# Optimization experiments

Hardware: AMD Instinct MI355X
Metric: run time of the kernel (lower is better)

The kernel has to match this reference:

```python
import jax, jax.numpy as jnp
import numpy as np


def setup_inputs() -> dict:
    key = jax.random.key(0)
    N0, N1, N2, E0, E1 = 40000, 8000, 2000, 128000, 32000
    IN, HID = 512, 256
    ks = iter(jax.random.split(key, 40))
    def nk():
        return next(ks)
    def lin_w(shape):
        fan_in = shape[1]
        return jax.random.uniform(nk(), shape, jnp.float32, -1.0, 1.0) / np.sqrt(fan_in)
    inp = {}
    inp["x"] = jax.random.normal(nk(), (N0, IN), jnp.float32)
    inp["ppr"] = jax.random.uniform(nk(), (N1, N1), jnp.float32) / N1  # ~row-stochastic PPR
    inp["src0"] = jax.random.randint(nk(), (E0,), 0, N0)
    inp["dst0"] = jax.random.randint(nk(), (E0,), 0, N1)
    inp["src1"] = jax.random.randint(nk(), (E1,), 0, N1)
    inp["dst1"] = jax.random.randint(nk(), (E1,), 0, N2)
    inp["n1"] = N1
    inp["n2"] = N2
    # SAGEConv layer 0 (in->hid) and layer 1 (hid->hid); lin_l has bias, lin_r does not (PyG default)
    inp["Wl0"] = lin_w((HID, IN)); inp["bl0"] = jnp.zeros((HID,), jnp.float32); inp["Wr0"] = lin_w((HID, IN))
    inp["Wl1"] = lin_w((HID, HID)); inp["bl1"] = jnp.zeros((HID,), jnp.float32); inp["Wr1"] = lin_w((HID, HID))
    # self.linear = [Linear(IN,IN)+ReLU, Linear(IN,HID)]
    inp["Wa"] = lin_w((IN, IN)); inp["ba"] = jnp.zeros((IN,), jnp.float32)
    inp["Wb"] = lin_w((HID, IN)); inp["bb"] = jnp.zeros((HID,), jnp.float32)
    # lin1 / lin2 (no bias)
    inp["W1"] = lin_w((HID, HID)); inp["W2"] = lin_w((HID, HID))
    # proj = MLP(HID, HID, HID)
    inp["Wp1"] = lin_w((HID, HID)); inp["bp1"] = jnp.zeros((HID,), jnp.float32)
    inp["Wp2"] = lin_w((HID, HID)); inp["bp2"] = jnp.zeros((HID,), jnp.float32)
    # clf = MLP(HID, 32, 1)
    inp["Wc1"] = lin_w((32, HID)); inp["bc1"] = jnp.zeros((32,), jnp.float32)
    inp["Wc2"] = lin_w((1, 32)); inp["bc2"] = jnp.zeros((1,), jnp.float32)
    return inp


def reference(x, ppr, Wl0, bl0, Wr0, Wl1, bl1, Wr1, Wa, ba, Wb, bb,
              W1, W2, Wp1, bp1, Wp2, bp2, Wc1, bc1, Wc2, bc2,
              src0, dst0, src1, dst1, n1, n2):
    EPS = 1e-12
    def l2n(v):
        return v / jnp.maximum(jnp.linalg.norm(v, axis=-1, keepdims=True), EPS)
    def sage(h_src, h_tgt, src, dst, Wl, bl, Wr, n_tgt):
        msg = h_src[src]  # [E, d] gather
        s = jax.ops.segment_sum(msg, dst, num_segments=n_tgt)
        cnt = jax.ops.segment_sum(jnp.ones((dst.shape[0],), h_src.dtype), dst, num_segments=n_tgt)
        agg = s / jnp.maximum(cnt, 1.0)[:, None]  # scatter-mean
        return agg @ Wl.T + bl + h_tgt @ Wr.T
    # --- GraphSAGE encoder (eval mode: dropout no-op) ---
    h = x
    h = sage(h, h[:n1], src0, dst0, Wl0, bl0, Wr0, n1)
    h = jax.nn.relu(h)
    h = sage(h, h[:n2], src1, dst1, Wl1, bl1, Wr1, n2)
    ebds = jax.nn.log_softmax(h, axis=-1)  # output_type 'ebds' != 'ebd' -> log_softmax path
    # --- divergence loss ---
    o1 = l2n(ebds @ W1.T)
    o2 = l2n(ebds @ W2.T)
    div_loss = jnp.mean(jnp.sum((o1 - o2) ** 2, axis=-1))
    # --- PPR branch ---
    xp = ppr[:n1, :n1] @ x[:n1]              # [n1, IN]
    xp = jax.nn.relu(xp @ Wa.T + ba)         # linear[0]
    xp = ppr[:n2, :n2] @ xp[:n2]             # [n2, IN]
    xp = xp @ Wb.T + bb                      # linear[1] -> [n2, HID]
    g1 = l2n(ebds)
    g2 = l2n(xp)
    def proj(v):
        return jax.nn.relu(v @ Wp1.T + bp1) @ Wp2.T + bp2
    def clf(v):
        return jax.nn.relu(v @ Wc1.T + bc1) @ Wc2.T + bc2
    l1 = clf(proj(g1))  # [n2, 1]
    l2_ = clf(proj(g2))  # [n2, 1]
    logits_pair = jnp.concatenate([l1, l2_], axis=-1)  # [n2, 2]
    return logits_pair, div_loss
```

## Files before the change

kernel.cpp:

```cpp
#include <hip/hip_runtime.h>


typedef unsigned short ushort;
typedef __attribute__((ext_vector_type(8))) short short8;
typedef __attribute__((ext_vector_type(4))) float float4v;
typedef __attribute__((ext_vector_type(4))) float f32x4;
typedef __attribute__((ext_vector_type(2))) float f32x2;
typedef __attribute__((ext_vector_type(8))) unsigned short us8;
typedef __attribute__((ext_vector_type(4))) unsigned short us4;
typedef __attribute__((ext_vector_type(2))) unsigned short us2;

__device__ __forceinline__ ushort bf16_rne(float v) {
    unsigned u = __float_as_uint(v);
    u += 0x7fffu + ((u >> 16) & 1u);
    return (ushort)(u >> 16);
}
__device__ __forceinline__ float bf16_f32(ushort h) {
    return __uint_as_float((unsigned)h << 16);
}

constexpr long ZCNT0 = 0;
constexpr long ZCNT1 = 8000;
constexpr long ELL0  = 10240;
constexpr long ELL1  = 522240;
constexpr long H1F   = 650240;
constexpr long H2F   = 2714624;
constexpr long DIVCF = 3238912;
constexpr long XPBF  = 4287488;
constexpr long PB2   = 4811776;
constexpr long PART  = 5860352;
constexpr long FEND  = 10054656;
constexpr long U_PPRB  = 0;
constexpr long U_PPR2B = 16777216;
constexpr long U_XTB   = 20971520;
constexpr long U_XPATB = 25165824;
constexpr long U_A0    = 26214400;
constexpr long U_A1    = 38600704;
constexpr long U_ESPL  = 40697856;
constexpr long U_XPS   = 41746432;
constexpr long U_SPLT  = 43843584;
constexpr long U_TSPL  = 45940736;
constexpr long U_WC0   = 48037888;
constexpr long U_WC1   = 48431104;
constexpr long U_BD    = 48693248;
constexpr long U_WAD   = 48955392;
constexpr long U_WBD   = 49479680;
constexpr long U_WP1D  = 49741824;
constexpr long U_WP2D  = 49872896;
constexpr long U_XB    = 50003968;

struct GemmDesc {
    const ushort* A; const ushort* B;
    float* Cf; ushort* Cs; ushort* Ct;
    const float* bias;
    int K, lda, ldb, ldc;
    int ldso, nsplit, msplit, ldt;
    int gx, gy, kchunk;
    long slabsize;
    int flags;
};

__device__ __forceinline__ void run_gemm(const GemmDesc& d, int f,
                                         ushort* As, ushort* Bs)
{
    const int tid = threadIdx.x;
    const int lane = tid & 63, wave = tid >> 6;
    const int wm = (wave >> 1) * 64, wn = (wave & 1) * 64;
    const int lr = lane & 15, quad = lane >> 4;

    int per = d.gx * d.gy;
    int z = f / per;
    int rem = f - z * per;
    if (d.flags & 8) {
        int c = rem & 7, j = rem >> 3;
        rem = c * (per >> 3) + j;
    }
    int by = rem / d.gx, bx = rem - by * d.gx;
    const int bm = by * 128, bn = bx * 128;
    const int kbeg = z * d.kchunk;
    int kend = kbeg + d.kchunk; if (kend > d.K) kend = d.K;

    float4v acc[4][4] = {{{0.f, 0.f, 0.f, 0.f}}};

    for (int k0 = kbeg; k0 < kend; k0 += 128) {
#pragma unroll
        for (int issue = 0; issue < 8; ++issue) {
            int c = issue * 256 + tid;
            int r = c >> 4, p = c & 15;
            int kk = (p ^ (r & 15)) * 8;
            const ushort* ga = d.A + (long)(bm + r) * d.lda + k0 + kk;
            const ushort* gb = d.B + (long)(bn + r) * d.ldb + k0 + kk;
            __builtin_amdgcn_global_load_lds(
                (const __attribute__((address_space(1))) unsigned int*)ga,
                (__attribute__((address_space(3))) unsigned int*)&As[c * 8], 16, 0, 0);
            __builtin_amdgcn_global_load_lds(
                (const __attribute__((address_space(1))) unsigned int*)gb,
                (__attribute__((address_space(3))) unsigned int*)&Bs[c * 8], 16, 0, 0);
        }
        __syncthreads();

#pragma unroll
        for (int s = 0; s < 4; ++s) {
            short8 af[4], bf[4];
#pragma unroll
            for (int i = 0; i < 4; ++i) {
                int ra = wm + i * 16 + lr;
                af[i] = *(const short8*)&As[ra * 128 + (((s * 4 + quad) ^ (ra & 15)) * 8)];
                int rb = wn + i * 16 + lr;
                bf[i] = *(const short8*)&Bs[rb * 128 + (((s * 4 + quad) ^ (rb & 15)) * 8)];
            }
#pragma unroll
            for (int i = 0; i < 4; ++i)
#pragma unroll
                for (int j = 0; j < 4; ++j)
                    acc[i][j] = __builtin_amdgcn_mfma_f32_16x16x32_bf16(
                        af[i], bf[j], acc[i][j], 0, 0, 0);
        }
        __syncthreads();
    }

    if (d.flags & 16) {
        float* Cz = d.Cf + (long)z * d.slabsize;
#pragma unroll
        for (int i = 0; i < 4; ++i) {
            int row0 = bm + wm + i * 16 + quad * 4;
#pragma unroll
            for (int j = 0; j < 4; ++j) {
                int col = bn + wn + j * 16 + lr;
#pragma unroll
                for (int r = 0; r < 4; ++r)
                    Cz[(long)(row0 + r) * d.ldc + col] = acc[i][j][r];
            }
        }
        return;
    }

#pragma unroll
    for (int i = 0; i < 4; ++i) {
        int row0 = bm + wm + i * 16 + quad * 4;
#pragma unroll
        for (int j = 0; j < 4; ++j) {
            int col = bn + wn + j * 16 + lr;
            float bv = d.bias ? d.bias[col] : 0.f;
            us4 tp;
#pragma unroll
            for (int r = 0; r < 4; ++r) {
                int row = row0 + r;
                float v = acc[i][j][r] + bv;
                if (d.flags & 1) v = fmaxf(v, 0.f);
                if (d.Cf) d.Cf[(long)row * d.ldc + col] = v;
                if (d.Cs && row < d.msplit) {
                    if (d.flags & 2) {
                        ushort h = bf16_rne(v);
                        d.Cs[(long)row * d.ldso + col] = h;
                        d.Cs[(long)row * d.ldso + d.nsplit + col] = bf16_rne(v - bf16_f32(h));
                    } else {
                        d.Cs[(long)row * d.ldso + col] = bf16_rne(v);
                    }
                }
                if (d.flags & 4) tp[r] = bf16_rne(v);
            }
            if (d.flags & 4)
                *(us4*)&d.Ct[(long)col * d.ldt + row0] = tp;
        }
    }
}

__device__ __forceinline__ void reduce_body(
    const float* __restrict__ part, ushort* __restrict__ outs,
    long i, long n, int S)
{
    if (i >= n) return;
    float s = 0.f;
    for (int k = 0; k < S; ++k) s += part[(long)k * n + i];
    int r = (int)(i >> 9), c = (int)(i & 511);
    ushort h = bf16_rne(s);
    outs[(long)r * 1024 + c] = h;
    outs[(long)r * 1024 + 512 + c] = bf16_rne(s - bf16_f32(h));
}

__global__ __launch_bounds__(256) void gemm_one(GemmDesc d)
{
    __shared__ ushort As[16384];
    __shared__ ushort Bs[16384];
    run_gemm(d, blockIdx.x, As, Bs);
}

__global__ __launch_bounds__(256) void gemm_dual(GemmDesc d0, int n0, GemmDesc d1)
{
    __shared__ ushort As[16384];
    __shared__ ushort Bs[16384];
    int f = blockIdx.x;
    if (f < n0) run_gemm(d0, f, As, Bs);
    else        run_gemm(d1, f - n0, As, Bs);
}

__global__ __launch_bounds__(256) void reduce_split(
    const float* __restrict__ part, ushort* __restrict__ outs, long n, int S)
{
    reduce_body(part, outs, (long)blockIdx.x * 256 + threadIdx.x, n, S);
}

__global__ __launch_bounds__(256) void aggred(
    const float* __restrict__ h, const int* __restrict__ ell,
    const int* __restrict__ cnt, ushort* __restrict__ a1,
    const float* __restrict__ part, ushort* __restrict__ outs)
{
    __shared__ float pl[4][256];
    int b = blockIdx.x, t = threadIdx.x;
    if (b >= 2048) {
        reduce_body(part, outs, (long)(b - 2048) * 256 + t, 1048576L, 4);
        return;
    }
    int d = b;
    int w = t >> 6, lane = t & 63;
    int k = (d < 2000) ? min(cnt[d], 64) : 0;
    f32x4 s = {0.f, 0.f, 0.f, 0.f};
    int co = lane * 4;
    int j = w;
    for (; j + 12 < k; j += 16) {
        int e0 = ell[d + 2000 * j],        e1 = ell[d + 2000 * (j + 4)];
        int e2 = ell[d + 2000 * (j + 8)],  e3 = ell[d + 2000 * (j + 12)];
        f32x4 v0 = *(const f32x4*)&h[(long)e0 * 256 + co];
        f32x4 v1 = *(const f32x4*)&h[(long)e1 * 256 + co];
        f32x4 v2 = *(const f32x4*)&h[(long)e2 * 256 + co];
        f32x4 v3 = *(const f32x4*)&h[(long)e3 * 256 + co];
        s += v0; s += v1; s += v2; s += v3;
    }
    for (; j < k; j += 4)
        s += *(const f32x4*)&h[(long)ell[d + 2000 * j] * 256 + co];
#pragma unroll
    for (int q = 0; q < 4; ++q) pl[w][co + q] = s[q];
    __syncthreads();
    float inv = 1.f / fmaxf((float)k, 1.f);
    float a = (pl[0][t] + pl[1][t] + pl[2][t] + pl[3][t]) * inv;
    ushort hi = bf16_rne(a);
    long ro = (long)d * 1024;
    a1[ro + 512 + t] = hi;
    a1[ro + 768 + t] = bf16_rne(a - bf16_f32(hi));
}

__global__ __launch_bounds__(256) void prep(
    const float* __restrict__ ppr, const float* __restrict__ x,
    const float* __restrict__ Wr0, const float* __restrict__ Wl0,
    const float* __restrict__ Wr1, const float* __restrict__ Wl1,
    const float* __restrict__ W1,  const float* __restrict__ W2,
    const float* __restrict__ Wa,  const float* __restrict__ Wb,
    const float* __restrict__ Wp1, const float* __restrict__ Wp2,
    ushort* __restrict__ uws, int* __restrict__ iws, float* __restrict__ outloss)
{
    __shared__ float tsm[32][33];
    int b = blockIdx.x, t = threadIdx.x;

    if (b < 40) {
        int idx = b * 256 + t;
        if (idx < 10000) iws[idx] = 0;
        if (idx == 10000) *outloss = 0.f;
        return;
    }
    if (b < 296) {
        int b2 = b - 40;
        int sec = b2 >> 5;
        const float *sa, *sb = nullptr; long dstoff; int N, KA, dA, KB = 0, dB = 0;
        switch (sec) {
            case 0: sa = Wr0; KA = 512; dA = 1; sb = Wl0; KB = 512; dB = 2;
                    dstoff = U_WC0; N = 256; break;
            case 1: sa = Wr1; KA = 256; dA = 2; sb = Wl1; KB = 256; dB = 2;
                    dstoff = U_WC1; N = 256; break;
            case 2: sa = W1;  KA = 256; dA = 2; dstoff = U_BD;          N = 256; break;
            case 3: sa = W2;  KA = 256; dA = 2; dstoff = U_BD + 131072; N = 256; break;
            case 4: sa = Wa;  KA = 512; dA = 2; dstoff = U_WAD;  N = 512; break;
            case 5: sa = Wb;  KA = 512; dA = 2; dstoff = U_WBD;  N = 256; break;
            case 6: sa = Wp1; KA = 256; dA = 2; dstoff = U_WP1D; N = 256; break;
            default: sa = Wp2; KA = 256; dA = 2; dstoff = U_WP2D; N = 256; break;
        }
        int kd = KA * dA + KB * dB;
        long totv = (long)N * kd / 2;
        for (long v = (long)(b2 & 31) * 256 + t; v < totv; v += 8192) {
            long idx = v * 2;
            int n = (int)(idx / kd), rem = (int)(idx % kd);
            f32x2 val;
            if (rem < KA * dA) {
                int sc = rem % KA;
                val = *(const f32x2*)&sa[(long)n * KA + sc];
            } else {
                int sc = (rem - KA * dA) % KB;
                val = *(const f32x2*)&sb[(long)n * KB + sc];
            }
            us2 o; o[0] = bf16_rne(val[0]); o[1] = bf16_rne(val[1]);
            *(us2*)&uws[dstoff + idx] = o;
        }
        return;
    }
    if (b < 8488) {
        int id = b - 296;
        int r = id >> 2, q = id & 3;
        bool live = r < 2000;
        const float* row = ppr + (long)r * 8000;
        int cbeg = q * 2048;
#pragma unroll
        for (int pass = 0; pass < 2; ++pass) {
            int c = cbeg + pass * 1024 + t * 4;
            f32x4 v = {0.f, 0.f, 0.f, 0.f};
            if (live && c < 8000) v = *(const f32x4*)(row + c);
            us4 u;
            u[0] = bf16_rne(v[0]); u[1] = bf16_rne(v[1]);
            u[2] = bf16_rne(v[2]); u[3] = bf16_rne(v[3]);
            *(us4*)&uws[U_PPRB + (long)r * 8192 + c] = u;
            if (c < 2048) {
                us4 w = u;
                if (c >= 2000) { w[0] = 0; w[1] = 0; w[2] = 0; w[3] = 0; }
                *(us4*)&uws[U_PPR2B + (long)r * 2048 + c] = w;
            }
        }
        return;
    }
    if (b < 12584) {
        int id = b - 8488;
        int c0 = (id & 15) * 32, r0 = (id >> 4) * 32;
        int tx = t & 31, ty = t >> 5;
#pragma unroll
        for (int k = 0; k < 32; k += 8) {
            int r = r0 + ty + k;
            tsm[ty + k][tx] = (r < 8000) ? x[(long)r * 512 + c0 + tx] : 0.f;
        }
        __syncthreads();
#pragma unroll
        for (int k = 0; k < 32; k += 8) {
            int c = c0 + ty + k;
            uws[U_XTB + (long)c * 8192 + r0 + tx] = bf16_rne(tsm[tx][ty + k]);
        }
        return;
    }
    {
        long vi = (long)(b - 12584) * 256 + t;
        for (; vi < 5120000; vi += 327680) {
            long gidx = vi * 4;
            f32x4 v = *(const f32x4*)&x[gidx];
            us4 u;
            u[0] = bf16_rne(v[0]); u[1] = bf16_rne(v[1]);
            u[2] = bf16_rne(v[2]); u[3] = bf16_rne(v[3]);
            *(us4*)&uws[U_XB + gidx] = u;
            long row = gidx >> 9;
            if (row < 8064) {
                int col = (int)(gidx & 511);
                *(us4*)&uws[U_A0 + row * 1536 + col] = u;
            }
        }
    }
}

__global__ __launch_bounds__(256) void ell_fill(
    const int* __restrict__ src0, const int* __restrict__ dst0,
    const int* __restrict__ src1, const int* __restrict__ dst1,
    int* __restrict__ cnt0, int* __restrict__ cnt1,
    int* __restrict__ ell0, int* __restrict__ ell1, int E0, int E1)
{
    int e = blockIdx.x * 256 + threadIdx.x;
    if (e < E0) {
        int d = dst0[e];
        int r = atomicAdd(&cnt0[d], 1);
        if (r < 64) ell0[d + 8000 * r] = src0[e];
    } else if (e < E0 + E1) {
        int e1 = e - E0;
        int d = dst1[e1];
        int r = atomicAdd(&cnt1[d], 1);
        if (r < 64) ell1[d + 2000 * r] = src1[e1];
    }
}

__global__ __launch_bounds__(256) void csr_agg0(
    const ushort* __restrict__ xb, const int* __restrict__ ell,
    const int* __restrict__ cnt, ushort* __restrict__ a0)
{
    __shared__ float part[4][512];
    int d = blockIdx.x, t = threadIdx.x;
    int w = t >> 6, lane = t & 63;
    int k = (d < 8000) ? min(cnt[d], 64) : 0;
    float s[8] = {0.f, 0.f, 0.f, 0.f, 0.f, 0.f, 0.f, 0.f};
    int co = lane * 8;
    int j = w;
    for (; j + 12 < k; j += 16) {
        int e0 = ell[d + 8000 * j],        e1 = ell[d + 8000 * (j + 4)];
        int e2 = ell[d + 8000 * (j + 8)],  e3 = ell[d + 8000 * (j + 12)];
        us8 v0 = *(const us8*)&xb[(long)e0 * 512 + co];
        us8 v1 = *(const us8*)&xb[(long)e1 * 512 + co];
        us8 v2 = *(const us8*)&xb[(long)e2 * 512 + co];
        us8 v3 = *(const us8*)&xb[(long)e3 * 512 + co];
#pragma unroll
        for (int q = 0; q < 8; ++q)
            s[q] += bf16_f32(v0[q]) + bf16_f32(v1[q]) +
                    bf16_f32(v2[q]) + bf16_f32(v3[q]);
    }
    for (; j < k; j += 4) {
        us8 v = *(const us8*)&xb[(long)ell[d + 8000 * j] * 512 + co];
#pragma unroll
        for (int q = 0; q < 8; ++q) s[q] += bf16_f32(v[q]);
    }
#pragma unroll
    for (int q = 0; q < 8; ++q) part[w][co + q] = s[q];
    __syncthreads();
    float inv = 1.f / fmaxf((float)k, 1.f);
    long ro = (long)d * 1536;
#pragma unroll
    for (int h = 0; h < 2; ++h) {
        int c = 2 * t + h;
        float a = (part[0][c] + part[1][c] + part[2][c] + part[3][c]) * inv;
        ushort hi = bf16_rne(a);
        a0[ro + 512 + c] = hi;
        a0[ro + 1024 + c] = bf16_rne(a - bf16_f32(hi));
    }
}

__global__ __launch_bounds__(256) void rowcombo1(
    const float* __restrict__ h2, ushort* __restrict__ espl,
    ushort* __restrict__ splt)
{
    __shared__ float red[256];
    int i = blockIdx.x, t = threadIdx.x;
    float v = h2[(long)i * 256 + t];
    red[t] = v;
    __syncthreads();
    for (int s = 128; s > 0; s >>= 1) {
        if (t < s) red[t] = fmaxf(red[t], red[t + s]);
        __syncthreads();
    }
    float m = red[0];
    __syncthreads();
    float e = expf(v - m);
    red[t] = e;
    __syncthreads();
    for (int s = 128; s > 0; s >>= 1) {
        if (t < s) red[t] += red[t + s];
        __syncthreads();
    }
    float eb = v - (m + logf(red[0]));
    ushort hh = bf16_rne(eb);
    espl[(long)i * 512 + t] = hh;
    espl[(long)i * 512 + 256 + t] = bf16_rne(eb - bf16_f32(hh));
    __syncthreads();
    red[t] = eb * eb;
    __syncthreads();
    for (int s = 128; s > 0; s >>= 1) {
        if (t < s) red[t] += red[t + s];
        __syncthreads();
    }
    float g = eb / fmaxf(sqrtf(red[0]), 1e-12f);
    ushort gh = bf16_rne(g);
    splt[(long)i * 512 + t] = gh;
    splt[(long)i * 512 + 256 + t] = bf16_rne(g - bf16_f32(gh));
}

__global__ __launch_bounds__(256) void rowcombo2(
    const float* __restrict__ xpb, ushort* __restrict__ splt)
{
    __shared__ float red[256];
    int i = blockIdx.x, t = threadIdx.x;
    float v = xpb[(long)i * 256 + t];
    red[t] = v * v;
    __syncthreads();
    for (int s = 128; s > 0; s >>= 1) {
        if (t < s) red[t] += red[t + s];
        __syncthreads();
    }
    float g = v / fmaxf(sqrtf(red[0]), 1e-12f);
    ushort gh = bf16_rne(g);
    long ro = (long)(2048 + i) * 512;
    splt[ro + t] = gh;
    splt[ro + 256 + t] = bf16_rne(g - bf16_f32(gh));
}

__global__ __launch_bounds__(256) void final_combo(
    const float* __restrict__ p, const float* __restrict__ Wc1,
    const float* __restrict__ bc1, const float* __restrict__ Wc2,
    const float* __restrict__ bc2, float* __restrict__ out,
    const float* __restrict__ divc, float scale)
{
    __shared__ float v[256];
    __shared__ float ps[8][33];
    __shared__ float hsum[32];
    __shared__ float r2[256];
    int b = blockIdx.x, t = threadIdx.x;
    if (b >= 4096) {
        int i = b - 4096;
        float a = divc[(long)i * 512 + t], bb = divc[(long)i * 512 + 256 + t];
        v[t] = a * a;
        r2[t] = bb * bb;
        __syncthreads();
        for (int s = 128; s > 0; s >>= 1) {
            if (t < s) { v[t] += v[t + s]; r2[t] += r2[t + s]; }
            __syncthreads();
        }
        float na = fmaxf(sqrtf(v[0]), 1e-12f);
        float nb = fmaxf(sqrtf(r2[0]), 1e-12f);
        __syncthreads();
        float d = a / na - bb / nb;
        v[t] = d * d;
        __syncthreads();
        for (int s = 128; s > 0; s >>= 1) {
            if (t < s) v[t] += v[t + s];
            __syncthreads();
        }
        if (t == 0) atomicAdd(&out[4000], v[0] * scale);
        return;
    }
    int half = b >> 11, i = b & 2047;
    if (i >= 2000) return;
    v[t] = p[(long)b * 256 + t];
    __syncthreads();
    int o = t & 31, ch = t >> 5;
    const float* w = Wc1 + (long)o * 256 + ch * 32;
    const float* vv = v + ch * 32;
    float s = 0.f;
#pragma unroll
    for (int k2 = 0; k2 < 32; ++k2) s += vv[k2] * w[k2];
    ps[ch][o] = s;
    __syncthreads();
    if (t < 32) {
        float a = bc1[t];
#pragma unroll
        for (int c = 0; c < 8; ++c) a += ps[c][t];
        a = fmaxf(a, 0.f);
        hsum[t] = a * Wc2[t];
    }
    __syncthreads();
    if (t == 0) {
        float s2 = bc2[0];
        for (int k2 = 0; k2 < 32; ++k2) s2 += hsum[k2];
        out[(long)i * 2 + half] = s2;
    }
}

extern "C" void kernel_launch(void* const* d_in, const int* in_sizes, int n_in,
                              void* d_out, int out_size, void* d_ws, size_t ws_size,
                              hipStream_t stream)
{
    constexpr int N2 = 2000;

    const float* x   = (const float*)d_in[0];
    const float* ppr = (const float*)d_in[1];
    const int* src0  = (const int*)d_in[2];
    const int* dst0  = (const int*)d_in[3];
    const int* src1  = (const int*)d_in[4];
    const int* dst1  = (const int*)d_in[5];
    const float* Wl0 = (const float*)d_in[8];
    const float* bl0 = (const float*)d_in[9];
    const float* Wr0 = (const float*)d_in[10];
    const float* Wl1 = (const float*)d_in[11];
    const float* bl1 = (const float*)d_in[12];
    const float* Wr1 = (const float*)d_in[13];
    const float* Wa  = (const float*)d_in[14];
    const float* ba  = (const float*)d_in[15];
    const float* Wb  = (const float*)d_in[16];
    const float* bb  = (const float*)d_in[17];
    const float* W1  = (const float*)d_in[18];
    const float* W2  = (const float*)d_in[19];
    const float* Wp1 = (const float*)d_in[20];
    const float* bp1 = (const float*)d_in[21];
    const float* Wp2 = (const float*)d_in[22];
    const float* bp2 = (const float*)d_in[23];
    const float* Wc1 = (const float*)d_in[24];
    const float* bc1 = (const float*)d_in[25];
    const float* Wc2 = (const float*)d_in[26];
    const float* bc2 = (const float*)d_in[27];

    const int E0 = in_sizes[2];
    const int E1 = in_sizes[4];

    float* out = (float*)d_out;
    float* ws  = (float*)d_ws;
    int*   iws = (int*)d_ws;
    ushort* uws = (ushort*)((char*)d_ws + FEND * sizeof(float));

    auto cdiv = [](int a, int b) { return (a + b - 1) / b; };

    GemmDesc z{};

    prep<<<13864, 256, 0, stream>>>(ppr, x, Wr0, Wl0, Wr1, Wl1, W1, W2,
                                    Wa, Wb, Wp1, Wp2, uws, iws, out + (long)N2 * 2);

    ell_fill<<<cdiv(E0 + E1, 256), 256, 0, stream>>>(
        src0, dst0, src1, dst1, iws + ZCNT0, iws + ZCNT1,
        iws + ELL0, iws + ELL1, E0, E1);

    csr_agg0<<<8064, 256, 0, stream>>>(uws + U_XB, iws + ELL0, iws + ZCNT0,
                                       uws + U_A0);

    GemmDesc dxp1 = z;
    dxp1.A = uws + U_PPRB; dxp1.B = uws + U_XTB; dxp1.Cf = ws + PART;
    dxp1.K = 8192; dxp1.lda = 8192; dxp1.ldb = 8192; dxp1.ldc = 512;
    dxp1.gx = 4; dxp1.gy = 16; dxp1.kchunk = 2048; dxp1.slabsize = 1048576;
    dxp1.flags = 16 | 8;
    GemmDesc dh1 = z;
    dh1.A = uws + U_A0; dh1.B = uws + U_WC0; dh1.Cf = ws + H1F;
    dh1.Cs = uws + U_A1; dh1.bias = bl0;
    dh1.K = 1536; dh1.lda = 1536; dh1.ldb = 1536; dh1.ldc = 256;
    dh1.ldso = 1024; dh1.nsplit = 256; dh1.msplit = 2048;
    dh1.gx = 2; dh1.gy = 63; dh1.kchunk = 1536; dh1.flags = 3;
    gemm_dual<<<382, 256, 0, stream>>>(dxp1, 256, dh1);

    aggred<<<6144, 256, 0, stream>>>(ws + H1F, iws + ELL1, iws + ZCNT1,
                                     uws + U_A1, ws + PART, uws + U_XPS);

    GemmDesc dxpa = z;
    dxpa.A = uws + U_XPS; dxpa.B = uws + U_WAD; dxpa.Ct = uws + U_XPATB;
    dxpa.bias = ba;
    dxpa.K = 1024; dxpa.lda = 1024; dxpa.ldb = 1024; dxpa.ldt = 2048;
    dxpa.gx = 4; dxpa.gy = 16; dxpa.kchunk = 1024; dxpa.flags = 1 | 4 | 8;
    GemmDesc dh2 = z;
    dh2.A = uws + U_A1; dh2.B = uws + U_WC1; dh2.Cf = ws + H2F; dh2.bias = bl1;
    dh2.K = 1024; dh2.lda = 1024; dh2.ldb = 1024; dh2.ldc = 256;
    dh2.gx = 2; dh2.gy = 16; dh2.kchunk = 1024; dh2.flags = 8;
    gemm_dual<<<96, 256, 0, stream>>>(dxpa, 64, dh2);

    rowcombo1<<<N2, 256, 0, stream>>>(ws + H2F, uws + U_ESPL, uws + U_SPLT);

    GemmDesc dxp2 = z;
    dxp2.A = uws + U_PPR2B; dxp2.B = uws + U_XPATB; dxp2.Cf = ws + PART;
    dxp2.K = 2048; dxp2.lda = 2048; dxp2.ldb = 2048; dxp2.ldc = 512;
    dxp2.gx = 4; dxp2.gy = 16; dxp2.kchunk = 1024; dxp2.slabsize = 1048576;
    dxp2.flags = 16 | 8;
    GemmDesc ddiv = z;
    ddiv.A = uws + U_ESPL; ddiv.B = uws + U_BD; ddiv.Cf = ws + DIVCF;
    ddiv.K = 512; ddiv.lda = 512; ddiv.ldb = 512; ddiv.ldc = 512;
    ddiv.gx = 4; ddiv.gy = 16; ddiv.kchunk = 512; ddiv.flags = 8;
    gemm_dual<<<192, 256, 0, stream>>>(dxp2, 128, ddiv);

    reduce_split<<<4096, 256, 0, stream>>>(ws + PART, uws + U_XPS, 1048576L, 2);

    GemmDesc dxpb = z;
    dxpb.A = uws + U_XPS; dxpb.B = uws + U_WBD; dxpb.Cf = ws + XPBF;
    dxpb.bias = bb;
    dxpb.K = 1024; dxpb.lda = 1024; dxpb.ldb = 1024; dxpb.ldc = 256;
    dxpb.gx = 2; dxpb.gy = 16; dxpb.kchunk = 1024; dxpb.flags = 8;
    gemm_one<<<32, 256, 0, stream>>>(dxpb);

    rowcombo2<<<N2, 256, 0, stream>>>(ws + XPBF, uws + U_SPLT);

    GemmDesc dp1 = z;
    dp1.A = uws + U_SPLT; dp1.B = uws + U_WP1D; dp1.Cs = uws + U_TSPL;
    dp1.bias = bp1;
    dp1.K = 512; dp1.lda = 512; dp1.ldb = 512;
    dp1.ldso = 512; dp1.nsplit = 256; dp1.msplit = 4096;
    dp1.gx = 2; dp1.gy = 32; dp1.kchunk = 512; dp1.flags = 1 | 2 | 8;
    gemm_one<<<64, 256, 0, stream>>>(dp1);

    GemmDesc dp2 = z;
    dp2.A = uws + U_TSPL; dp2.B = uws + U_WP2D; dp2.Cf = ws + PB2;
    dp2.bias = bp2;
    dp2.K = 512; dp2.lda = 512; dp2.ldb = 512; dp2.ldc = 256;
    dp2.gx = 2; dp2.gy = 32; dp2.kchunk = 512; dp2.flags = 8;
    gemm_one<<<64, 256, 0, stream>>>(dp2);

    final_combo<<<6096, 256, 0, stream>>>(ws + PB2, Wc1, bc1, Wc2, bc2, out,
                                          ws + DIVCF, 1.0f / N2);
}
```

Baseline: 672.5 us.

## Fuse launches: merge ELL fill into prep, fuse xpb GEMM with row L2 norm

Moves edge ELL construction into the prep kernel, replacing the count-zeroing blocks with a memset. Rewrites the xp@Wb GEMM as a 128x256 tile variant that computes the row L2 norm in its epilogue and writes split bf16 directly, removing rowcombo2 and the XPBF buffer. Pairs rowcombo1 with the second split-K reduction in one launch. Widens the reductions to 4-wide vectors and co-schedules the div GEMM with the normalized GEMM. The aim is fewer launches and less intermediate traffic, at the cost of less overlap: the dxp2 GEMM now runs alone and the fused GEMM uses one block per 128 rows.

New measurement: 694.2 us. +3.2%, slower.

```diff
diff --git a/kernel.cpp b/kernel.cpp
--- a/kernel.cpp
+++ b/kernel.cpp
@@ -26,7 +26,6 @@
 constexpr long H1F   = 650240;
 constexpr long H2F   = 2714624;
 constexpr long DIVCF = 3238912;
-constexpr long XPBF  = 4287488;
 constexpr long PB2   = 4811776;
 constexpr long PART  = 5860352;
 constexpr long FEND  = 10054656;
@@ -166,17 +165,118 @@
     }
 }
 
-__device__ __forceinline__ void reduce_body(
-    const float* __restrict__ part, ushort* __restrict__ outs,
-    long i, long n, int S)
-{
-    if (i >= n) return;
-    float s = 0.f;
-    for (int k = 0; k < S; ++k) s += part[(long)k * n + i];
-    int r = (int)(i >> 9), c = (int)(i & 511);
-    ushort h = bf16_rne(s);
-    outs[(long)r * 1024 + c] = h;
-    outs[(long)r * 1024 + 512 + c] = bf16_rne(s - bf16_f32(h));
+__device__ __forceinline__ void run_gemm_norm(const GemmDesc& d, int f,
+                                              ushort* As, ushort* Bs)
+{
+    const int tid = threadIdx.x;
+    const int lane = tid & 63, wave = tid >> 6;
+    const int wm = (wave >> 1) * 64, wn = (wave & 1) * 64;
+    const int lr = lane & 15, quad = lane >> 4;
+    const int bm = f * 128;
+
+    float4v acc[2][4][4] = {{{{0.f, 0.f, 0.f, 0.f}}}};
+
+#pragma unroll 2
+    for (int tile = 0; tile < 2; ++tile) {
+        for (int k0 = 0; k0 < d.K; k0 += 128) {
+#pragma unroll
+            for (int issue = 0; issue < 8; ++issue) {
+                int c = issue * 256 + tid;
+                int r = c >> 4, p = c & 15;
+                int kk = (p ^ (r & 15)) * 8;
+                const ushort* ga = d.A + (long)(bm + r) * d.lda + k0 + kk;
+                const ushort* gb = d.B + (long)(tile * 128 + r) * d.ldb + k0 + kk;
+                __builtin_amdgcn_global_load_lds(
+                    (const __attribute__((address_space(1))) unsigned int*)ga,
+                    (__attribute__((address_space(3))) unsigned int*)&As[c * 8], 16, 0, 0);
+                __builtin_amdgcn_global_load_lds(
+                    (const __attribute__((address_space(1))) unsigned int*)gb,
+                    (__attribute__((address_space(3))) unsigned int*)&Bs[c * 8], 16, 0, 0);
+            }
+            __syncthreads();
+#pragma unroll
+            for (int s = 0; s < 4; ++s) {
+                short8 af[4], bf[4];
+#pragma unroll
+                for (int i = 0; i < 4; ++i) {
+                    int ra = wm + i * 16 + lr;
+                    af[i] = *(const short8*)&As[ra * 128 + (((s * 4 + quad) ^ (ra & 15)) * 8)];
+                    int rb = wn + i * 16 + lr;
+                    bf[i] = *(const short8*)&Bs[rb * 128 + (((s * 4 + quad) ^ (rb & 15)) * 8)];
+                }
+#pragma unroll
+                for (int i = 0; i < 4; ++i)
+#pragma unroll
+                    for (int j = 0; j < 4; ++j)
+                        acc[tile][i][j] = __builtin_amdgcn_mfma_f32_16x16x32_bf16(
+                            af[i], bf[j], acc[tile][i][j], 0, 0, 0);
+            }
+            __syncthreads();
+        }
+    }
+
+    float* rs = (float*)As;
+    if (tid < 128) rs[tid] = 0.f;
+    __syncthreads();
+#pragma unroll
+    for (int i = 0; i < 4; ++i) {
+#pragma unroll
+        for (int r = 0; r < 4; ++r) {
+            int rl = wm + i * 16 + quad * 4 + r;
+            float p = 0.f;
+#pragma unroll
+            for (int j = 0; j < 4; ++j) {
+                int c0 = wn + j * 16 + lr;
+                float v0 = acc[0][i][j][r] + d.bias[c0];
+                float v1 = acc[1][i][j][r] + d.bias[128 + c0];
+                acc[0][i][j][r] = v0;
+                acc[1][i][j][r] = v1;
+                p += v0 * v0 + v1 * v1;
+            }
+            atomicAdd(&rs[rl], p);
+        }
+    }
+    __syncthreads();
+#pragma unroll
+    for (int i = 0; i < 4; ++i) {
+#pragma unroll
+        for (int r = 0; r < 4; ++r) {
+            int rl = wm + i * 16 + quad * 4 + r;
+            float inv = 1.f / fmaxf(sqrtf(rs[rl]), 1e-12f);
+            long ro = (long)(bm + rl) * 512;
+#pragma unroll
+            for (int j = 0; j < 4; ++j) {
+                int c0 = wn + j * 16 + lr;
+                float g0 = acc[0][i][j][r] * inv;
+                float g1 = acc[1][i][j][r] * inv;
+                ushort h0 = bf16_rne(g0), h1 = bf16_rne(g1);
+                d.Cs[ro + c0] = h0;
+                d.Cs[ro + 256 + c0] = bf16_rne(g0 - bf16_f32(h0));
+                d.Cs[ro + 128 + c0] = h1;
+                d.Cs[ro + 256 + 128 + c0] = bf16_rne(g1 - bf16_f32(h1));
+            }
+        }
+    }
+}
+
+__device__ __forceinline__ void reduce4_body(
+    const float* __restrict__ part, ushort* __restrict__ outs, long j, int S)
+{
+    if (j >= 262144) return;
+    long i4 = j * 4;
+    f32x4 s = {0.f, 0.f, 0.f, 0.f};
+    for (int k = 0; k < S; ++k)
+        s += *(const f32x4*)&part[(long)k * 1048576 + i4];
+    int r = (int)(i4 >> 9), c = (int)(i4 & 511);
+    us4 hi, lo;
+#pragma unroll
+    for (int q = 0; q < 4; ++q) {
+        ushort h = bf16_rne(s[q]);
+        hi[q] = h;
+        lo[q] = bf16_rne(s[q] - bf16_f32(h));
+    }
+    *(us4*)&outs[(long)r * 1024 + c] = hi;
+    *(us4*)&outs[(long)r * 1024 + 512 + c] = lo;
 }
 
 __global__ __launch_bounds__(256) void gemm_one(GemmDesc d)
@@ -192,13 +292,8 @@
     __shared__ ushort Bs[16384];
     int f = blockIdx.x;
     if (f < n0) run_gemm(d0, f, As, Bs);
-    else        run_gemm(d1, f - n0, As, Bs);
-}
-
-__global__ __launch_bounds__(256) void reduce_split(
-    const float* __restrict__ part, ushort* __restrict__ outs, long n, int S)
-{
-    reduce_body(part, outs, (long)blockIdx.x * 256 + threadIdx.x, n, S);
+    else if (d1.flags & 32) run_gemm_norm(d1, f - n0, As, Bs);
+    else run_gemm(d1, f - n0, As, Bs);
 }
 
 __global__ __launch_bounds__(256) void aggred(
@@ -209,7 +304,7 @@
     __shared__ float pl[4][256];
     int b = blockIdx.x, t = threadIdx.x;
     if (b >= 2048) {
-        reduce_body(part, outs, (long)(b - 2048) * 256 + t, 1048576L, 4);
+        reduce4_body(part, outs, (long)(b - 2048) * 256 + t, 4);
         return;
     }
     int d = b;
@@ -240,6 +335,51 @@
     a1[ro + 768 + t] = bf16_rne(a - bf16_f32(hi));
 }
 
+__global__ __launch_bounds__(256) void auxdual2(
+    const float* __restrict__ h2, ushort* __restrict__ espl,
+    ushort* __restrict__ splt,
+    const float* __restrict__ part, ushort* __restrict__ outs)
+{
+    __shared__ float red[256];
+    int b = blockIdx.x, t = threadIdx.x;
+    if (b >= 2000) {
+        reduce4_body(part, outs, (long)(b - 2000) * 256 + t, 2);
+        return;
+    }
+    int i = b;
+    float v = h2[(long)i * 256 + t];
+    red[t] = v;
+    __syncthreads();
+    for (int s = 128; s > 0; s >>= 1) {
+        if (t < s) red[t] = fmaxf(red[t], red[t + s]);
+        __syncthreads();
+    }
+    float m = red[0];
+    __syncthreads();
+    float e = expf(v - m);
+    red[t] = e;
+    __syncthreads();
+    for (int s = 128; s > 0; s >>= 1) {
+        if (t < s) red[t] += red[t + s];
+        __syncthreads();
+    }
+    float eb = v - (m + logf(red[0]));
+    ushort hh = bf16_rne(eb);
+    espl[(long)i * 512 + t] = hh;
+    espl[(long)i * 512 + 256 + t] = bf16_rne(eb - bf16_f32(hh));
+    __syncthreads();
+    red[t] = eb * eb;
+    __syncthreads();
+    for (int s = 128; s > 0; s >>= 1) {
+        if (t < s) red[t] += red[t + s];
+        __syncthreads();
+    }
+    float g = eb / fmaxf(sqrtf(red[0]), 1e-12f);
+    ushort gh = bf16_rne(g);
+    splt[(long)i * 512 + t] = gh;
+    splt[(long)i * 512 + 256 + t] = bf16_rne(g - bf16_f32(gh));
+}
+
 __global__ __launch_bounds__(256) void prep(
     const float* __restrict__ ppr, const float* __restrict__ x,
     const float* __restrict__ Wr0, const float* __restrict__ Wl0,
@@ -247,19 +387,37 @@
     const float* __restrict__ W1,  const float* __restrict__ W2,
     const float* __restrict__ Wa,  const float* __restrict__ Wb,
     const float* __restrict__ Wp1, const float* __restrict__ Wp2,
+    const int* __restrict__ src0, const int* __restrict__ dst0,
+    const int* __restrict__ src1, const int* __restrict__ dst1,
+    int E0, int E1,
     ushort* __restrict__ uws, int* __restrict__ iws, float* __restrict__ outloss)
 {
     __shared__ float tsm[32][33];
     int b = blockIdx.x, t = threadIdx.x;
-
-    if (b < 40) {
-        int idx = b * 256 + t;
-        if (idx < 10000) iws[idx] = 0;
-        if (idx == 10000) *outloss = 0.f;
-        return;
-    }
-    if (b < 296) {
-        int b2 = b - 40;
+    int nEll = (E0 + E1 + 255) >> 8;
+
+    if (b < nEll) {
+        int e = b * 256 + t;
+        if (e < E0) {
+            int d = dst0[e];
+            int r = atomicAdd(&iws[ZCNT0 + d], 1);
+            if (r < 64) iws[ELL0 + d + 8000 * r] = src0[e];
+        } else if (e < E0 + E1) {
+            int e1 = e - E0;
+            int d = dst1[e1];
+            int r = atomicAdd(&iws[ZCNT1 + d], 1);
+            if (r < 64) iws[ELL1 + d + 2000 * r] = src1[e1];
+        }
+        return;
+    }
+    int b1 = b - nEll;
+    if (b1 == 0) {
+        if (t == 0) outloss[0] = 0.f;
+        return;
+    }
+    b1 -= 1;
+    if (b1 < 256) {
+        int b2 = b1;
         int sec = b2 >> 5;
         const float *sa, *sb = nullptr; long dstoff; int N, KA, dA, KB = 0, dB = 0;
         switch (sec) {
@@ -292,9 +450,9 @@
         }
         return;
     }
-    if (b < 8488) {
-        int id = b - 296;
-        int r = id >> 2, q = id & 3;
+    b1 -= 256;
+    if (b1 < 8192) {
+        int r = b1 >> 2, q = b1 & 3;
         bool live = r < 2000;
         const float* row = ppr + (long)r * 8000;
         int cbeg = q * 2048;
@@ -315,9 +473,9 @@
         }
         return;
     }
-    if (b < 12584) {
-        int id = b - 8488;
-        int c0 = (id & 15) * 32, r0 = (id >> 4) * 32;
+    b1 -= 8192;
+    if (b1 < 4096) {
+        int c0 = (b1 & 15) * 32, r0 = (b1 >> 4) * 32;
         int tx = t & 31, ty = t >> 5;
 #pragma unroll
         for (int k = 0; k < 32; k += 8) {
@@ -332,8 +490,9 @@
         }
         return;
     }
+    b1 -= 4096;
     {
-        long vi = (long)(b - 12584) * 256 + t;
+        long vi = (long)b1 * 256 + t;
         for (; vi < 5120000; vi += 327680) {
             long gidx = vi * 4;
             f32x4 v = *(const f32x4*)&x[gidx];
@@ -347,25 +506,6 @@
                 *(us4*)&uws[U_A0 + row * 1536 + col] = u;
             }
         }
-    }
-}
-
-__global__ __launch_bounds__(256) void ell_fill(
-    const int* __restrict__ src0, const int* __restrict__ dst0,
-    const int* __restrict__ src1, const int* __restrict__ dst1,
-    int* __restrict__ cnt0, int* __restrict__ cnt1,
-    int* __restrict__ ell0, int* __restrict__ ell1, int E0, int E1)
-{
-    int e = blockIdx.x * 256 + threadIdx.x;
-    if (e < E0) {
-        int d = dst0[e];
-        int r = atomicAdd(&cnt0[d], 1);
-        if (r < 64) ell0[d + 8000 * r] = src0[e];
-    } else if (e < E0 + E1) {
-        int e1 = e - E0;
-        int d = dst1[e1];
-        int r = atomicAdd(&cnt1[d], 1);
-        if (r < 64) ell1[d + 2000 * r] = src1[e1];
     }
 }
 
@@ -410,64 +550,6 @@
         a0[ro + 512 + c] = hi;
         a0[ro + 1024 + c] = bf16_rne(a - bf16_f32(hi));
     }
-}
-
-__global__ __launch_bounds__(256) void rowcombo1(
-    const float* __restrict__ h2, ushort* __restrict__ espl,
-    ushort* __restrict__ splt)
-{
-    __shared__ float red[256];
-    int i = blockIdx.x, t = threadIdx.x;
-    float v = h2[(long)i * 256 + t];
-    red[t] = v;
-    __syncthreads();
-    for (int s = 128; s > 0; s >>= 1) {
-        if (t < s) red[t] = fmaxf(red[t], red[t + s]);
-        __syncthreads();
-    }
-    float m = red[0];
-    __syncthreads();
-    float e = expf(v - m);
-    red[t] = e;
-    __syncthreads();
-    for (int s = 128; s > 0; s >>= 1) {
-        if (t < s) red[t] += red[t + s];
-        __syncthreads();
-    }
-    float eb = v - (m + logf(red[0]));
-    ushort hh = bf16_rne(eb);
-    espl[(long)i * 512 + t] = hh;
-    espl[(long)i * 512 + 256 + t] = bf16_rne(eb - bf16_f32(hh));
-    __syncthreads();
-    red[t] = eb * eb;
-    __syncthreads();
-    for (int s = 128; s > 0; s >>= 1) {
-        if (t < s) red[t] += red[t + s];
-        __syncthreads();
-    }
-    float g = eb / fmaxf(sqrtf(red[0]), 1e-12f);
-    ushort gh = bf16_rne(g);
-    splt[(long)i * 512 + t] = gh;
-    splt[(long)i * 512 + 256 + t] = bf16_rne(g - bf16_f32(gh));
-}
-
-__global__ __launch_bounds__(256) void rowcombo2(
-    const float* __restrict__ xpb, ushort* __restrict__ splt)
-{
-    __shared__ float red[256];
-    int i = blockIdx.x, t = threadIdx.x;
-    float v = xpb[(long)i * 256 + t];
-    red[t] = v * v;
-    __syncthreads();
-    for (int s = 128; s > 0; s >>= 1) {
-        if (t < s) red[t] += red[t + s];
-        __syncthreads();
-    }
-    float g = v / fmaxf(sqrtf(red[0]), 1e-12f);
-    ushort gh = bf16_rne(g);
-    long ro = (long)(2048 + i) * 512;
-    splt[ro + t] = gh;
-    splt[ro + 256 + t] = bf16_rne(g - bf16_f32(gh));
 }
 
 __global__ __launch_bounds__(256) void final_combo(
@@ -572,16 +654,16 @@
     int*   iws = (int*)d_ws;
     ushort* uws = (ushort*)((char*)d_ws + FEND * sizeof(float));
 
-    auto cdiv = [](int a, int b) { return (a + b - 1) / b; };
-
     GemmDesc z{};
 
-    prep<<<13864, 256, 0, stream>>>(ppr, x, Wr0, Wl0, Wr1, Wl1, W1, W2,
-                                    Wa, Wb, Wp1, Wp2, uws, iws, out + (long)N2 * 2);
-
-    ell_fill<<<cdiv(E0 + E1, 256), 256, 0, stream>>>(
-        src0, dst0, src1, dst1, iws + ZCNT0, iws + ZCNT1,
-        iws + ELL0, iws + ELL1, E0, E1);
+    hipMemsetAsync(iws, 0, 10240 * sizeof(int), stream);
+
+    int nEll = (E0 + E1 + 255) / 256;
+    int prepGrid = nEll + 1 + 256 + 8192 + 4096 + 1280;
+    prep<<<prepGrid, 256, 0, stream>>>(ppr, x, Wr0, Wl0, Wr1, Wl1, W1, W2,
+                                       Wa, Wb, Wp1, Wp2,
+                                       src0, dst0, src1, dst1, E0, E1,
+                                       uws, iws, out + (long)N2 * 2);
 
     csr_agg0<<<8064, 256, 0, stream>>>(uws + U_XB, iws + ELL0, iws + ZCNT0,
                                        uws + U_A0);
@@ -599,7 +681,7 @@
     dh1.gx = 2; dh1.gy = 63; dh1.kchunk = 1536; dh1.flags = 3;
     gemm_dual<<<382, 256, 0, stream>>>(dxp1, 256, dh1);
 
-    aggred<<<6144, 256, 0, stream>>>(ws + H1F, iws + ELL1, iws + ZCNT1,
+    aggred<<<3072, 256, 0, stream>>>(ws + H1F, iws + ELL1, iws + ZCNT1,
                                      uws + U_A1, ws + PART, uws + U_XPS);
 
     GemmDesc dxpa = z;
@@ -613,29 +695,27 @@
     dh2.gx = 2; dh2.gy = 16; dh2.kchunk = 1024; dh2.flags = 8;
     gemm_dual<<<96, 256, 0, stream>>>(dxpa, 64, dh2);
 
-    rowcombo1<<<N2, 256, 0, stream>>>(ws + H2F, uws + U_ESPL, uws + U_SPLT);
-
     GemmDesc dxp2 = z;
     dxp2.A = uws + U_PPR2B; dxp2.B = uws + U_XPATB; dxp2.Cf = ws + PART;
     dxp2.K = 2048; dxp2.lda = 2048; dxp2.ldb = 2048; dxp2.ldc = 512;
     dxp2.gx = 4; dxp2.gy = 16; dxp2.kchunk = 1024; dxp2.slabsize = 1048576;
     dxp2.flags = 16 | 8;
+    gemm_one<<<128, 256, 0, stream>>>(dxp2);
+
+    auxdual2<<<3024, 256, 0, stream>>>(ws + H2F, uws + U_ESPL, uws + U_SPLT,
+                                       ws + PART, uws + U_XPS);
+
     GemmDesc ddiv = z;
     ddiv.A = uws + U_ESPL; ddiv.B = uws + U_BD; ddiv.Cf = ws + DIVCF;
     ddiv.K = 512; ddiv.lda = 512; ddiv.ldb = 512; ddiv.ldc = 512;
     ddiv.gx = 4; ddiv.gy = 16; ddiv.kchunk = 512; ddiv.flags = 8;
-    gemm_dual<<<192, 256, 0, stream>>>(dxp2, 128, ddiv);
-
-    reduce_split<<<4096, 256, 0, stream>>>(ws + PART, uws + U_XPS, 1048576L, 2);
-
-    GemmDesc dxpb = z;
-    dxpb.A = uws + U_XPS; dxpb.B = uws + U_WBD; dxpb.Cf = ws + XPBF;
-    dxpb.bias = bb;
-    dxpb.K = 1024; dxpb.lda = 1024; dxpb.ldb = 1024; dxpb.ldc = 256;
-    dxpb.gx = 2; dxpb.gy = 16; dxpb.kchunk = 1024; dxpb.flags = 8;
-    gemm_one<<<32, 256, 0, stream>>>(dxpb);
-
-    rowcombo2<<<N2, 256, 0, stream>>>(ws + XPBF, uws + U_SPLT);
+    GemmDesc dnorm = z;
+    dnorm.A = uws + U_XPS; dnorm.B = uws + U_WBD;
+    dnorm.Cs = uws + U_SPLT + (long)2048 * 512;
+    dnorm.bias = bb;
+    dnorm.K = 1024; dnorm.lda = 1024; dnorm.ldb = 1024;
+    dnorm.flags = 32;
+    gemm_dual<<<80, 256, 0, stream>>>(ddiv, 64, dnorm);
 
     GemmDesc dp1 = z;
     dp1.A = uws + U_SPLT; dp1.B = uws + U_WP1D; dp1.Cs = uws + U_TSPL;
```
